# Performance work log

Measured on AMD Instinct MI355X. Metric: run time of the kernel, lower is better.

## Reference

```python
import jax, jax.numpy as jnp
import numpy as np

HEADS = 16
DIM_HEAD = 64


def setup_inputs() -> dict:
    key = jax.random.key(0)
    k1, k2, k3, k4 = jax.random.split(key, 4)
    b, n, d = 2, 2048, 1024
    x = jax.random.normal(k1, (b, n, d), dtype=jnp.float32)
    attn_mask = jax.random.randint(k2, (b, n, n), 0, 2) == 1  # bool mask, True = masked out
    Wqkv = jax.random.normal(k3, (d, 3 * HEADS * DIM_HEAD), dtype=jnp.float32) * (d ** -0.5)
    Wfc = jax.random.normal(k4, (HEADS * DIM_HEAD, d), dtype=jnp.float32) * ((HEADS * DIM_HEAD) ** -0.5)
    return {"x": x, "attn_mask": attn_mask, "Wqkv": Wqkv, "Wfc": Wfc}


def reference(x, attn_mask, Wqkv, Wfc):
    b, n, d = x.shape
    h, dh = HEADS, DIM_HEAD
    qkv = x @ Wqkv  # [b, n, 3*h*dh]
    q, k, v = jnp.split(qkv, 3, axis=-1)
    def to_heads(t):
        return t.reshape(b, n, h, dh).transpose(0, 2, 1, 3)  # b h n d
    q, k, v = to_heads(q), to_heads(k), to_heads(v)
    # NOTE: original divides by scale = dim_head**-0.5, i.e. multiplies by sqrt(dim_head)
    scale = dh ** (-0.5)
    scores = jnp.einsum('bhqd,bhkd->bhqk', q, k) / scale
    scores = jnp.where(attn_mask[:, None, :, :], jnp.float32(-1e9), scores)
    attn = jax.nn.softmax(scores, axis=-1)
    context = jnp.einsum('bhqk,bhkd->bhqd', attn, v)  # b h n dh
    context = context.transpose(0, 2, 1, 3).reshape(b, n, h * dh)
    out = context @ Wfc
    return out, attn
```

## Files before the change

### kernel.cpp

```cpp
#include <hip/hip_runtime.h>

#define HEADS  16
#define DH     64
#define NBATCH 2
#define SEQ    2048
#define DMODEL 1024

typedef unsigned short u16;
typedef unsigned int   u32;
typedef unsigned long long u64;

typedef __attribute__((ext_vector_type(8))) short short8v;
typedef __attribute__((ext_vector_type(4))) float floatx4;

__device__ __forceinline__ u16 f2bf(float f) {
    u32 u = __float_as_uint(f);
    return (u16)((u + 0x7fffu + ((u >> 16) & 1u)) >> 16);
}
__device__ __forceinline__ float bf2f(u16 h) {
    return __uint_as_float(((u32)h) << 16);
}

__global__ void k_split(const float* __restrict__ in, u16* __restrict__ hi,
                        u16* __restrict__ lo, int n4) {
    int i = blockIdx.x * blockDim.x + threadIdx.x;
    if (i >= n4) return;
    float4 v = reinterpret_cast<const float4*>(in)[i];
    ushort4 hv, lv;
    hv.x = f2bf(v.x); hv.y = f2bf(v.y); hv.z = f2bf(v.z); hv.w = f2bf(v.w);
    lv.x = f2bf(v.x - bf2f(hv.x));
    lv.y = f2bf(v.y - bf2f(hv.y));
    lv.z = f2bf(v.z - bf2f(hv.z));
    lv.w = f2bf(v.w - bf2f(hv.w));
    reinterpret_cast<ushort4*>(hi)[i] = hv;
    reinterpret_cast<ushort4*>(lo)[i] = lv;
}

__global__ void k_tsplit(const float* __restrict__ in, u16* __restrict__ hiT,
                         u16* __restrict__ loT, int R, int C, int write_lo) {
    __shared__ float tile[64][65];
    int c0 = blockIdx.x * 64, r0 = blockIdx.y * 64;
    int t = threadIdx.x;
    int lr = t >> 4;
    int lc = (t & 15) * 4;
    for (int i = 0; i < 4; i++) {
        int r = lr + i * 16;
        float4 v = *reinterpret_cast<const float4*>(&in[(size_t)(r0 + r) * C + c0 + lc]);
        tile[r][lc] = v.x; tile[r][lc + 1] = v.y; tile[r][lc + 2] = v.z; tile[r][lc + 3] = v.w;
    }
    __syncthreads();
    for (int i = 0; i < 4; i++) {
        int cc = lr + i * 16;
        float vs0 = tile[lc + 0][cc], vs1 = tile[lc + 1][cc];
        float vs2 = tile[lc + 2][cc], vs3 = tile[lc + 3][cc];
        ushort4 hv, lv;
        hv.x = f2bf(vs0); hv.y = f2bf(vs1); hv.z = f2bf(vs2); hv.w = f2bf(vs3);
        *reinterpret_cast<ushort4*>(&hiT[(size_t)(c0 + cc) * R + r0 + lc]) = hv;
        if (write_lo) {
            lv.x = f2bf(vs0 - bf2f(hv.x)); lv.y = f2bf(vs1 - bf2f(hv.y));
            lv.z = f2bf(vs2 - bf2f(hv.z)); lv.w = f2bf(vs3 - bf2f(hv.w));
            *reinterpret_cast<ushort4*>(&loT[(size_t)(c0 + cc) * R + r0 + lc]) = lv;
        }
    }
}

__global__ void k_maskpack(const int* __restrict__ m, u64* __restrict__ bits) {
    int i = blockIdx.x * 256 + threadIdx.x;
    u64 b = __ballot(m[i] != 0);
    if ((threadIdx.x & 63) == 0) bits[((u32)i) >> 6] = b;
}

__global__ __launch_bounds__(256, 2) void k_qkv(
    const u16* __restrict__ xh, const u16* __restrict__ xl,
    const u16* __restrict__ whT, const u16* __restrict__ wlT,
    u16* __restrict__ qh, u16* __restrict__ ql,
    u16* __restrict__ kh, u16* __restrict__ kl,
    u16* __restrict__ vt)
{
    __shared__ __attribute__((aligned(16))) u16 sA[2][128][72];
    __shared__ __attribute__((aligned(16))) u16 sB[2][128][72];
    int n0 = blockIdx.x * 128;
    int m0 = blockIdx.y * 128;
    bool is_v = (n0 >= 2 * DMODEL);
    int tid = threadIdx.x;
    int wave = tid >> 6, lane = tid & 63;
    int wm = (wave >> 1) * 64, wn = (wave & 1) * 64;
    int lrow = lane & 15, lgrp = lane >> 4;

    floatx4 acc[4][4];
    for (int i = 0; i < 4; i++) for (int j = 0; j < 4; j++) acc[i][j] = (floatx4){0.f, 0.f, 0.f, 0.f};

    int sr = tid >> 1;
    int sc = (tid & 1) * 32;

    for (int k0 = 0; k0 < DMODEL; k0 += 64) {
        const u16* pxh = xh + (size_t)(m0 + sr) * DMODEL + k0 + sc;
        const u16* pwh = whT + (size_t)(n0 + sr) * DMODEL + k0 + sc;
        for (int i = 0; i < 4; i++) {
            *reinterpret_cast<int4*>(&sA[0][sr][sc + i * 8]) = *reinterpret_cast<const int4*>(pxh + i * 8);
            *reinterpret_cast<int4*>(&sB[0][sr][sc + i * 8]) = *reinterpret_cast<const int4*>(pwh + i * 8);
        }
        if (!is_v) {
            const u16* pxl = xl + (size_t)(m0 + sr) * DMODEL + k0 + sc;
            const u16* pwl = wlT + (size_t)(n0 + sr) * DMODEL + k0 + sc;
            for (int i = 0; i < 4; i++) {
                *reinterpret_cast<int4*>(&sA[1][sr][sc + i * 8]) = *reinterpret_cast<const int4*>(pxl + i * 8);
                *reinterpret_cast<int4*>(&sB[1][sr][sc + i * 8]) = *reinterpret_cast<const int4*>(pwl + i * 8);
            }
        }
        __syncthreads();
        for (int ks = 0; ks < 2; ks++) {
            short8v ah[4], bh_[4], al[4], bl_[4];
            for (int i = 0; i < 4; i++) {
                ah[i]  = *reinterpret_cast<const short8v*>(&sA[0][wm + i * 16 + lrow][ks * 32 + lgrp * 8]);
                bh_[i] = *reinterpret_cast<const short8v*>(&sB[0][wn + i * 16 + lrow][ks * 32 + lgrp * 8]);
            }
            if (!is_v) {
                for (int i = 0; i < 4; i++) {
                    al[i]  = *reinterpret_cast<const short8v*>(&sA[1][wm + i * 16 + lrow][ks * 32 + lgrp * 8]);
                    bl_[i] = *reinterpret_cast<const short8v*>(&sB[1][wn + i * 16 + lrow][ks * 32 + lgrp * 8]);
                }
            }
            for (int i = 0; i < 4; i++)
                for (int j = 0; j < 4; j++) {
                    acc[i][j] = __builtin_amdgcn_mfma_f32_16x16x32_bf16(ah[i], bh_[j], acc[i][j], 0, 0, 0);
                    if (!is_v) {
                        acc[i][j] = __builtin_amdgcn_mfma_f32_16x16x32_bf16(ah[i], bl_[j], acc[i][j], 0, 0, 0);
                        acc[i][j] = __builtin_amdgcn_mfma_f32_16x16x32_bf16(al[i], bh_[j], acc[i][j], 0, 0, 0);
                    }
                }
        }
        __syncthreads();
    }
    for (int j = 0; j < 4; j++) {
        int c = n0 + wn + j * 16 + lrow;
        int sel = c >> 10;
        int hcol = c & 1023;
        int hh = hcol >> 6, d = hcol & 63;
        for (int i = 0; i < 4; i++) {
            int mbase = m0 + wm + i * 16 + lgrp * 4;
            int bb = mbase >> 11;
            int nn = mbase & 2047;
            int bh = bb * HEADS + hh;
            if (sel == 2) {
                ushort4 pv;
                pv.x = f2bf(acc[i][j][0]); pv.y = f2bf(acc[i][j][1]);
                pv.z = f2bf(acc[i][j][2]); pv.w = f2bf(acc[i][j][3]);
                *reinterpret_cast<ushort4*>(&vt[((size_t)bh * DH + d) * SEQ + nn]) = pv;
            } else {
                u16* oh = (sel == 0) ? qh : kh;
                u16* ol = (sel == 0) ? ql : kl;
                float sc8 = (sel == 0) ? 8.0f : 1.0f;
                for (int r = 0; r < 4; r++) {
                    float v = acc[i][j][r] * sc8;
                    u16 hv = f2bf(v);
                    u16 lv = f2bf(v - bf2f(hv));
                    size_t addr = ((size_t)bh * SEQ + nn + r) * DH + d;
                    oh[addr] = hv; ol[addr] = lv;
                }
            }
        }
    }
}

__global__ __launch_bounds__(256, 2) void k_attn(
    const u16* __restrict__ qh, const u16* __restrict__ ql,
    const u16* __restrict__ kh, const u16* __restrict__ kl,
    const u16* __restrict__ vt, const u32* __restrict__ mb,
    float* __restrict__ attn, u16* __restrict__ ctx)
{
    __shared__ __attribute__((aligned(16))) u16 sK[2][128][72];
    __shared__ __attribute__((aligned(16))) u16 sV[64][136];
    __shared__ __attribute__((aligned(16))) u16 sP[64][136];
    __shared__ u32 sMask[64][4];
    __shared__ float sML[2][4][64];

    int bh = blockIdx.y;
    int b = bh >> 4, hh = bh & 15;
    int q0 = blockIdx.x * 64;
    int tid = threadIdx.x, wave = tid >> 6, lane = tid & 63;
    int lrow = lane & 15, lgrp = lane >> 4;
    int sr = tid >> 1, scol = (tid & 1) * 32;
    int mr = tid >> 2, mw = tid & 3;

    short8v qfh[4][2], qfl[4][2];
    for (int nt = 0; nt < 4; nt++) {
        int qr = q0 + nt * 16 + lrow;
        const u16* pq = qh + ((size_t)bh * SEQ + qr) * DH + lgrp * 8;
        const u16* pl = ql + ((size_t)bh * SEQ + qr) * DH + lgrp * 8;
        for (int ks = 0; ks < 2; ks++) {
            qfh[nt][ks] = *reinterpret_cast<const short8v*>(pq + ks * 32);
            qfl[nt][ks] = *reinterpret_cast<const short8v*>(pl + ks * 32);
        }
    }

#define STAGE_K_MASK() do { \
        const u16* ph_ = kh + ((size_t)bh * SEQ + kt * 128 + sr) * DH + scol; \
        const u16* pl_ = kl + ((size_t)bh * SEQ + kt * 128 + sr) * DH + scol; \
        for (int i_ = 0; i_ < 4; i_++) { \
            *reinterpret_cast<int4*>(&sK[0][sr][scol + i_ * 8]) = *reinterpret_cast<const int4*>(ph_ + i_ * 8); \
            *reinterpret_cast<int4*>(&sK[1][sr][scol + i_ * 8]) = *reinterpret_cast<const int4*>(pl_ + i_ * 8); \
        } \
        sMask[mr][mw] = mb[((size_t)b * SEQ + q0 + mr) * 64 + kt * 4 + mw]; \
    } while (0)

#define COMPUTE_ST() do { \
        for (int mt_ = 0; mt_ < 2; mt_++) for (int nt_ = 0; nt_ < 4; nt_++) sacc[mt_][nt_] = (floatx4){0.f,0.f,0.f,0.f}; \
        for (int ks_ = 0; ks_ < 2; ks_++) { \
            short8v kfh[2], kfl[2]; \
            for (int mt_ = 0; mt_ < 2; mt_++) { \
                kfh[mt_] = *reinterpret_cast<const short8v*>(&sK[0][wave * 32 + mt_ * 16 + lrow][ks_ * 32 + lgrp * 8]); \
                kfl[mt_] = *reinterpret_cast<const short8v*>(&sK[1][wave * 32 + mt_ * 16 + lrow][ks_ * 32 + lgrp * 8]); \
            } \
            for (int mt_ = 0; mt_ < 2; mt_++) for (int nt_ = 0; nt_ < 4; nt_++) { \
                sacc[mt_][nt_] = __builtin_amdgcn_mfma_f32_16x16x32_bf16(kfh[mt_], qfh[nt_][ks_], sacc[mt_][nt_], 0, 0, 0); \
                sacc[mt_][nt_] = __builtin_amdgcn_mfma_f32_16x16x32_bf16(kfh[mt_], qfl[nt_][ks_], sacc[mt_][nt_], 0, 0, 0); \
                sacc[mt_][nt_] = __builtin_amdgcn_mfma_f32_16x16x32_bf16(kfl[mt_], qfh[nt_][ks_], sacc[mt_][nt_], 0, 0, 0); \
            } \
        } \
    } while (0)

    float m_run[4], l_run[4];
    for (int nt = 0; nt < 4; nt++) { m_run[nt] = -3.0e38f; l_run[nt] = 0.f; }

    for (int kt = 0; kt < 16; kt++) {
        STAGE_K_MASK();
        __syncthreads();
        floatx4 sacc[2][4];
        COMPUTE_ST();
        for (int nt = 0; nt < 4; nt++) {
            u32 mwrd = sMask[nt * 16 + lrow][wave];
            float s[8];
            for (int mt = 0; mt < 2; mt++)
                for (int r = 0; r < 4; r++) {
                    int bit = mt * 16 + lgrp * 4 + r;
                    s[mt * 4 + r] = ((mwrd >> bit) & 1u) ? -1e9f : sacc[mt][nt][r];
                }
            float tmax = s[0];
            for (int u = 1; u < 8; u++) tmax = fmaxf(tmax, s[u]);
            tmax = fmaxf(tmax, __shfl_xor(tmax, 16));
            tmax = fmaxf(tmax, __shfl_xor(tmax, 32));
            float mn = fmaxf(m_run[nt], tmax);
            float ssum = 0.f;
            for (int u = 0; u < 8; u++) ssum += __expf(s[u] - mn);
            ssum += __shfl_xor(ssum, 16);
            ssum += __shfl_xor(ssum, 32);
            l_run[nt] = l_run[nt] * __expf(m_run[nt] - mn) + ssum;
            m_run[nt] = mn;
        }
        __syncthreads();
    }
    if (lane < 16) {
        for (int nt = 0; nt < 4; nt++) {
            sML[0][wave][nt * 16 + lane] = m_run[nt];
            sML[1][wave][nt * 16 + lane] = l_run[nt];
        }
    }
    __syncthreads();
    float m_fin[4], rl[4];
    for (int nt = 0; nt < 4; nt++) {
        int qr = nt * 16 + lrow;
        float m4 = sML[0][0][qr];
        for (int w = 1; w < 4; w++) m4 = fmaxf(m4, sML[0][w][qr]);
        float ls = 0.f;
        for (int w = 0; w < 4; w++) ls += sML[1][w][qr] * __expf(sML[0][w][qr] - m4);
        m_fin[nt] = m4;
        rl[nt] = 1.0f / ls;
    }

    floatx4 cacc[4];
    for (int j = 0; j < 4; j++) cacc[j] = (floatx4){0.f, 0.f, 0.f, 0.f};

    for (int kt = 0; kt < 16; kt++) {
        STAGE_K_MASK();
        {
            int vd = tid >> 2, vq = (tid & 3) * 32;
            const u16* pv = vt + ((size_t)bh * DH + vd) * SEQ + kt * 128 + vq;
            for (int i = 0; i < 4; i++)
                *reinterpret_cast<int4*>(&sV[vd][vq + i * 8]) = *reinterpret_cast<const int4*>(pv + i * 8);
        }
        __syncthreads();
        floatx4 sacc[2][4];
        COMPUTE_ST();
        for (int nt = 0; nt < 4; nt++) {
            u32 mwrd = sMask[nt * 16 + lrow][wave];
            int qr = q0 + nt * 16 + lrow;
            for (int mt = 0; mt < 2; mt++) {
                float4 pf;
                float* pp = &pf.x;
                for (int r = 0; r < 4; r++) {
                    int bit = mt * 16 + lgrp * 4 + r;
                    float sv = ((mwrd >> bit) & 1u) ? -1e9f : sacc[mt][nt][r];
                    pp[r] = __expf(sv - m_fin[nt]) * rl[nt];
                }
                int kc = kt * 128 + wave * 32 + mt * 16 + lgrp * 4;
                *reinterpret_cast<float4*>(&attn[((size_t)bh * SEQ + qr) * SEQ + kc]) = pf;
                ushort4 pb;
                pb.x = f2bf(pp[0]); pb.y = f2bf(pp[1]); pb.z = f2bf(pp[2]); pb.w = f2bf(pp[3]);
                *reinterpret_cast<ushort4*>(&sP[nt * 16 + lrow][wave * 32 + mt * 16 + lgrp * 4]) = pb;
            }
        }
        __syncthreads();
        for (int ks = 0; ks < 4; ks++) {
            short8v pfrag = *reinterpret_cast<const short8v*>(&sP[wave * 16 + lrow][ks * 32 + lgrp * 8]);
            for (int j = 0; j < 4; j++) {
                short8v vfrag = *reinterpret_cast<const short8v*>(&sV[j * 16 + lrow][ks * 32 + lgrp * 8]);
                cacc[j] = __builtin_amdgcn_mfma_f32_16x16x32_bf16(pfrag, vfrag, cacc[j], 0, 0, 0);
            }
        }
        __syncthreads();
    }
    for (int j = 0; j < 4; j++) {
        int d = j * 16 + lrow;
        for (int r = 0; r < 4; r++) {
            int nn = q0 + wave * 16 + lgrp * 4 + r;
            ctx[((size_t)b * SEQ + nn) * DMODEL + hh * 64 + d] = f2bf(cacc[j][r]);
        }
    }
#undef STAGE_K_MASK
#undef COMPUTE_ST
}

__global__ __launch_bounds__(256, 2) void k_out(
    const u16* __restrict__ ctx, const u16* __restrict__ wfcT, float* __restrict__ out)
{
    __shared__ __attribute__((aligned(16))) u16 sA[128][72];
    __shared__ __attribute__((aligned(16))) u16 sB[128][72];
    int n0 = blockIdx.x * 128;
    int m0 = blockIdx.y * 128;
    int tid = threadIdx.x;
    int wave = tid >> 6, lane = tid & 63;
    int wm = (wave >> 1) * 64, wn = (wave & 1) * 64;
    int lrow = lane & 15, lgrp = lane >> 4;

    floatx4 acc[4][4];
    for (int i = 0; i < 4; i++) for (int j = 0; j < 4; j++) acc[i][j] = (floatx4){0.f, 0.f, 0.f, 0.f};

    int sr = tid >> 1;
    int sc = (tid & 1) * 32;

    for (int k0 = 0; k0 < DMODEL; k0 += 64) {
        const u16* pa = ctx + (size_t)(m0 + sr) * DMODEL + k0 + sc;
        const u16* pb = wfcT + (size_t)(n0 + sr) * DMODEL + k0 + sc;
        for (int i = 0; i < 4; i++) {
            *reinterpret_cast<int4*>(&sA[sr][sc + i * 8]) = *reinterpret_cast<const int4*>(pa + i * 8);
            *reinterpret_cast<int4*>(&sB[sr][sc + i * 8]) = *reinterpret_cast<const int4*>(pb + i * 8);
        }
        __syncthreads();
        for (int ks = 0; ks < 2; ks++) {
            short8v af[4], bf[4];
            for (int i = 0; i < 4; i++) {
                af[i] = *reinterpret_cast<const short8v*>(&sA[wm + i * 16 + lrow][ks * 32 + lgrp * 8]);
                bf[i] = *reinterpret_cast<const short8v*>(&sB[wn + i * 16 + lrow][ks * 32 + lgrp * 8]);
            }
            for (int i = 0; i < 4; i++)
                for (int j = 0; j < 4; j++)
                    acc[i][j] = __builtin_amdgcn_mfma_f32_16x16x32_bf16(af[i], bf[j], acc[i][j], 0, 0, 0);
        }
        __syncthreads();
    }
    for (int i = 0; i < 4; i++)
        for (int j = 0; j < 4; j++)
            for (int r = 0; r < 4; r++) {
                int m = m0 + wm + i * 16 + lgrp * 4 + r;
                int c = n0 + wn + j * 16 + lrow;
                out[(size_t)m * DMODEL + c] = acc[i][j][r];
            }
}

extern "C" void kernel_launch(void* const* d_in, const int* in_sizes, int n_in,
                              void* d_out, int out_size, void* d_ws, size_t ws_size,
                              hipStream_t stream) {
    const float* x    = (const float*)d_in[0];
    const int*   mask = (const int*)d_in[1];
    const float* wqkv = (const float*)d_in[2];
    const float* wfc  = (const float*)d_in[3];

    float* out  = (float*)d_out;
    float* attn = out + (size_t)NBATCH * SEQ * DMODEL;

    u16* xh   = (u16*)d_ws;
    u16* xl   = xh + 4194304;
    u16* whT  = xl + 4194304;
    u16* wlT  = whT + 3145728;
    u16* wfcT = wlT + 3145728;
    u16* qh   = wfcT + 1048576;
    u16* ql   = qh + 4194304;
    u16* kh   = ql + 4194304;
    u16* kl   = kh + 4194304;
    u16* vt   = kl + 4194304;
    u32* mbits = (u32*)(vt + 4194304);
    u16* ctx  = xh;

    k_split<<<4096, 256, 0, stream>>>(x, xh, xl, 4194304 / 4);
    k_tsplit<<<dim3(48, 16), 256, 0, stream>>>(wqkv, whT, wlT, 1024, 3072, 1);
    k_tsplit<<<dim3(16, 16), 256, 0, stream>>>(wfc, wfcT, (u16*)nullptr, 1024, 1024, 0);
    k_maskpack<<<32768, 256, 0, stream>>>(mask, (u64*)mbits);
    k_qkv<<<dim3(24, 32), 256, 0, stream>>>(xh, xl, whT, wlT, qh, ql, kh, kl, vt);
    k_attn<<<dim3(32, 32), 256, 0, stream>>>(qh, ql, kh, kl, vt, mbits, attn, ctx);
    k_out<<<dim3(8, 32), 256, 0, stream>>>(ctx, wfcT, out);
}
```

Baseline: 444.1 us.

## Prefetch tiles into registers, shrink attention K tile, switch softmax to exp2

Adds register-staged prefetch of the next K-slice in the QKV and output GEMMs so global loads overlap MFMA work. The attention kernel moves to 64-key tiles with double-buffered K and mask in shared memory, and loads V fragments straight from global memory into registers instead of staging them in LDS. Softmax folds log2(e) into the Q scale and uses exp2 with a precomputed log-sum, which removes the per-element reciprocal. Masked scores now become -3e38 instead of -1e9, so a fully masked row would behave differently. Register pressure rises and LDS use drops.

```diff
diff --git a/kernel.cpp b/kernel.cpp
--- a/kernel.cpp
+++ b/kernel.cpp
@@ -93,22 +93,39 @@
     int sr = tid >> 1;
     int sc = (tid & 1) * 32;
 
+    int4 rah[4], rbh[4], ral[4], rbl[4];
+
+#define QKV_ISSUE(K0) do { \
+        const u16* pxh_ = xh + (size_t)(m0 + sr) * DMODEL + (K0) + sc; \
+        const u16* pwh_ = whT + (size_t)(n0 + sr) * DMODEL + (K0) + sc; \
+        for (int i_ = 0; i_ < 4; i_++) { \
+            rah[i_] = *reinterpret_cast<const int4*>(pxh_ + i_ * 8); \
+            rbh[i_] = *reinterpret_cast<const int4*>(pwh_ + i_ * 8); \
+        } \
+        if (!is_v) { \
+            const u16* pxl_ = xl + (size_t)(m0 + sr) * DMODEL + (K0) + sc; \
+            const u16* pwl_ = wlT + (size_t)(n0 + sr) * DMODEL + (K0) + sc; \
+            for (int i_ = 0; i_ < 4; i_++) { \
+                ral[i_] = *reinterpret_cast<const int4*>(pxl_ + i_ * 8); \
+                rbl[i_] = *reinterpret_cast<const int4*>(pwl_ + i_ * 8); \
+            } \
+        } \
+    } while (0)
+
+    QKV_ISSUE(0);
     for (int k0 = 0; k0 < DMODEL; k0 += 64) {
-        const u16* pxh = xh + (size_t)(m0 + sr) * DMODEL + k0 + sc;
-        const u16* pwh = whT + (size_t)(n0 + sr) * DMODEL + k0 + sc;
         for (int i = 0; i < 4; i++) {
-            *reinterpret_cast<int4*>(&sA[0][sr][sc + i * 8]) = *reinterpret_cast<const int4*>(pxh + i * 8);
-            *reinterpret_cast<int4*>(&sB[0][sr][sc + i * 8]) = *reinterpret_cast<const int4*>(pwh + i * 8);
+            *reinterpret_cast<int4*>(&sA[0][sr][sc + i * 8]) = rah[i];
+            *reinterpret_cast<int4*>(&sB[0][sr][sc + i * 8]) = rbh[i];
         }
         if (!is_v) {
-            const u16* pxl = xl + (size_t)(m0 + sr) * DMODEL + k0 + sc;
-            const u16* pwl = wlT + (size_t)(n0 + sr) * DMODEL + k0 + sc;
             for (int i = 0; i < 4; i++) {
-                *reinterpret_cast<int4*>(&sA[1][sr][sc + i * 8]) = *reinterpret_cast<const int4*>(pxl + i * 8);
-                *reinterpret_cast<int4*>(&sB[1][sr][sc + i * 8]) = *reinterpret_cast<const int4*>(pwl + i * 8);
-            }
-        }
-        __syncthreads();
+                *reinterpret_cast<int4*>(&sA[1][sr][sc + i * 8]) = ral[i];
+                *reinterpret_cast<int4*>(&sB[1][sr][sc + i * 8]) = rbl[i];
+            }
+        }
+        __syncthreads();
+        if (k0 + 64 < DMODEL) QKV_ISSUE(k0 + 64);
         for (int ks = 0; ks < 2; ks++) {
             short8v ah[4], bh_[4], al[4], bl_[4];
             for (int i = 0; i < 4; i++) {
@@ -132,6 +149,7 @@
         }
         __syncthreads();
     }
+#undef QKV_ISSUE
     for (int j = 0; j < 4; j++) {
         int c = n0 + wn + j * 16 + lrow;
         int sel = c >> 10;
@@ -150,7 +168,7 @@
             } else {
                 u16* oh = (sel == 0) ? qh : kh;
                 u16* ol = (sel == 0) ? ql : kl;
-                float sc8 = (sel == 0) ? 8.0f : 1.0f;
+                float sc8 = (sel == 0) ? 11.5415603f : 1.0f;
                 for (int r = 0; r < 4; r++) {
                     float v = acc[i][j][r] * sc8;
                     u16 hv = f2bf(v);
@@ -169,19 +187,20 @@
     const u16* __restrict__ vt, const u32* __restrict__ mb,
     float* __restrict__ attn, u16* __restrict__ ctx)
 {
-    __shared__ __attribute__((aligned(16))) u16 sK[2][128][72];
-    __shared__ __attribute__((aligned(16))) u16 sV[64][136];
-    __shared__ __attribute__((aligned(16))) u16 sP[64][136];
-    __shared__ u32 sMask[64][4];
+    __shared__ __attribute__((aligned(16))) u16 sKh[2][64][72];
+    __shared__ __attribute__((aligned(16))) u16 sKl[2][64][72];
+    __shared__ __attribute__((aligned(16))) u16 sP[64][72];
+    __shared__ u32 sMask[2][64][2];
     __shared__ float sML[2][4][64];
 
     int bh = blockIdx.y;
-    int b = bh >> 4, hh = bh & 15;
+    int b = bh >> 4;
     int q0 = blockIdx.x * 64;
     int tid = threadIdx.x, wave = tid >> 6, lane = tid & 63;
     int lrow = lane & 15, lgrp = lane >> 4;
-    int sr = tid >> 1, scol = (tid & 1) * 32;
-    int mr = tid >> 2, mw = tid & 3;
+    int sr4 = tid >> 2, sc4 = (tid & 3) * 16;
+    int mbit = (wave & 1) * 16 + lgrp * 4;
+    int mwsel = wave >> 1;
 
     short8v qfh[4][2], qfl[4][2];
     for (int nt = 0; nt < 4; nt++) {
@@ -194,62 +213,73 @@
         }
     }
 
-#define STAGE_K_MASK() do { \
-        const u16* ph_ = kh + ((size_t)bh * SEQ + kt * 128 + sr) * DH + scol; \
-        const u16* pl_ = kl + ((size_t)bh * SEQ + kt * 128 + sr) * DH + scol; \
-        for (int i_ = 0; i_ < 4; i_++) { \
-            *reinterpret_cast<int4*>(&sK[0][sr][scol + i_ * 8]) = *reinterpret_cast<const int4*>(ph_ + i_ * 8); \
-            *reinterpret_cast<int4*>(&sK[1][sr][scol + i_ * 8]) = *reinterpret_cast<const int4*>(pl_ + i_ * 8); \
-        } \
-        sMask[mr][mw] = mb[((size_t)b * SEQ + q0 + mr) * 64 + kt * 4 + mw]; \
+    int4 hh0, hh1, ll0, ll1;
+    u32 mv = 0;
+
+#define K_ISSUE(KT) do { \
+        const u16* ph_ = kh + ((size_t)bh * SEQ + (KT) * 64 + sr4) * DH + sc4; \
+        const u16* pl_ = kl + ((size_t)bh * SEQ + (KT) * 64 + sr4) * DH + sc4; \
+        hh0 = *reinterpret_cast<const int4*>(ph_); \
+        hh1 = *reinterpret_cast<const int4*>(ph_ + 8); \
+        ll0 = *reinterpret_cast<const int4*>(pl_); \
+        ll1 = *reinterpret_cast<const int4*>(pl_ + 8); \
+        if (tid < 128) mv = mb[((size_t)b * SEQ + q0 + (tid >> 1)) * 64 + (KT) * 2 + (tid & 1)]; \
     } while (0)
 
-#define COMPUTE_ST() do { \
-        for (int mt_ = 0; mt_ < 2; mt_++) for (int nt_ = 0; nt_ < 4; nt_++) sacc[mt_][nt_] = (floatx4){0.f,0.f,0.f,0.f}; \
+#define K_WRITE(B_) do { \
+        *reinterpret_cast<int4*>(&sKh[B_][sr4][sc4])     = hh0; \
+        *reinterpret_cast<int4*>(&sKh[B_][sr4][sc4 + 8]) = hh1; \
+        *reinterpret_cast<int4*>(&sKl[B_][sr4][sc4])     = ll0; \
+        *reinterpret_cast<int4*>(&sKl[B_][sr4][sc4 + 8]) = ll1; \
+        if (tid < 128) sMask[B_][tid >> 1][tid & 1] = mv; \
+    } while (0)
+
+#define COMPUTE_ST(CUR) do { \
+        for (int nt_ = 0; nt_ < 4; nt_++) sacc[nt_] = (floatx4){0.f, 0.f, 0.f, 0.f}; \
         for (int ks_ = 0; ks_ < 2; ks_++) { \
-            short8v kfh[2], kfl[2]; \
-            for (int mt_ = 0; mt_ < 2; mt_++) { \
-                kfh[mt_] = *reinterpret_cast<const short8v*>(&sK[0][wave * 32 + mt_ * 16 + lrow][ks_ * 32 + lgrp * 8]); \
-                kfl[mt_] = *reinterpret_cast<const short8v*>(&sK[1][wave * 32 + mt_ * 16 + lrow][ks_ * 32 + lgrp * 8]); \
-            } \
-            for (int mt_ = 0; mt_ < 2; mt_++) for (int nt_ = 0; nt_ < 4; nt_++) { \
-                sacc[mt_][nt_] = __builtin_amdgcn_mfma_f32_16x16x32_bf16(kfh[mt_], qfh[nt_][ks_], sacc[mt_][nt_], 0, 0, 0); \
-                sacc[mt_][nt_] = __builtin_amdgcn_mfma_f32_16x16x32_bf16(kfh[mt_], qfl[nt_][ks_], sacc[mt_][nt_], 0, 0, 0); \
-                sacc[mt_][nt_] = __builtin_amdgcn_mfma_f32_16x16x32_bf16(kfl[mt_], qfh[nt_][ks_], sacc[mt_][nt_], 0, 0, 0); \
+            short8v kfh_ = *reinterpret_cast<const short8v*>(&sKh[CUR][wave * 16 + lrow][ks_ * 32 + lgrp * 8]); \
+            short8v kfl_ = *reinterpret_cast<const short8v*>(&sKl[CUR][wave * 16 + lrow][ks_ * 32 + lgrp * 8]); \
+            for (int nt_ = 0; nt_ < 4; nt_++) { \
+                sacc[nt_] = __builtin_amdgcn_mfma_f32_16x16x32_bf16(kfh_, qfh[nt_][ks_], sacc[nt_], 0, 0, 0); \
+                sacc[nt_] = __builtin_amdgcn_mfma_f32_16x16x32_bf16(kfh_, qfl[nt_][ks_], sacc[nt_], 0, 0, 0); \
+                sacc[nt_] = __builtin_amdgcn_mfma_f32_16x16x32_bf16(kfl_, qfh[nt_][ks_], sacc[nt_], 0, 0, 0); \
             } \
         } \
     } while (0)
 
     float m_run[4], l_run[4];
-    for (int nt = 0; nt < 4; nt++) { m_run[nt] = -3.0e38f; l_run[nt] = 0.f; }
-
-    for (int kt = 0; kt < 16; kt++) {
-        STAGE_K_MASK();
-        __syncthreads();
-        floatx4 sacc[2][4];
-        COMPUTE_ST();
+    for (int nt = 0; nt < 4; nt++) { m_run[nt] = -1.0e38f; l_run[nt] = 0.f; }
+
+    K_ISSUE(0);
+    K_WRITE(0);
+    __syncthreads();
+    for (int kt = 0; kt < 32; kt++) {
+        int cur = kt & 1;
+        bool pf = kt < 31;
+        if (pf) K_ISSUE(kt + 1);
+        floatx4 sacc[4];
+        COMPUTE_ST(cur);
         for (int nt = 0; nt < 4; nt++) {
-            u32 mwrd = sMask[nt * 16 + lrow][wave];
-            float s[8];
-            for (int mt = 0; mt < 2; mt++)
-                for (int r = 0; r < 4; r++) {
-                    int bit = mt * 16 + lgrp * 4 + r;
-                    s[mt * 4 + r] = ((mwrd >> bit) & 1u) ? -1e9f : sacc[mt][nt][r];
-                }
-            float tmax = s[0];
-            for (int u = 1; u < 8; u++) tmax = fmaxf(tmax, s[u]);
+            u32 nw = ~sMask[cur][nt * 16 + lrow][mwsel];
+            float sm[4];
+            for (int r = 0; r < 4; r++)
+                sm[r] = ((nw >> (mbit + r)) & 1u) ? sacc[nt][r] : -3.0e38f;
+            float tmax = fmaxf(fmaxf(sm[0], sm[1]), fmaxf(sm[2], sm[3]));
             tmax = fmaxf(tmax, __shfl_xor(tmax, 16));
             tmax = fmaxf(tmax, __shfl_xor(tmax, 32));
             float mn = fmaxf(m_run[nt], tmax);
             float ssum = 0.f;
-            for (int u = 0; u < 8; u++) ssum += __expf(s[u] - mn);
+            for (int r = 0; r < 4; r++)
+                ssum += exp2f(sm[r] - mn);
             ssum += __shfl_xor(ssum, 16);
             ssum += __shfl_xor(ssum, 32);
-            l_run[nt] = l_run[nt] * __expf(m_run[nt] - mn) + ssum;
+            l_run[nt] = l_run[nt] * exp2f(m_run[nt] - mn) + ssum;
             m_run[nt] = mn;
         }
-        __syncthreads();
-    }
+        if (pf) K_WRITE((kt + 1) & 1);
+        __syncthreads();
+    }
+
     if (lane < 16) {
         for (int nt = 0; nt < 4; nt++) {
             sML[0][wave][nt * 16 + lane] = m_run[nt];
@@ -257,59 +287,60 @@
         }
     }
     __syncthreads();
-    float m_fin[4], rl[4];
+    float Cn[4];
     for (int nt = 0; nt < 4; nt++) {
         int qr = nt * 16 + lrow;
         float m4 = sML[0][0][qr];
         for (int w = 1; w < 4; w++) m4 = fmaxf(m4, sML[0][w][qr]);
         float ls = 0.f;
-        for (int w = 0; w < 4; w++) ls += sML[1][w][qr] * __expf(sML[0][w][qr] - m4);
-        m_fin[nt] = m4;
-        rl[nt] = 1.0f / ls;
+        for (int w = 0; w < 4; w++) ls += sML[1][w][qr] * exp2f(sML[0][w][qr] - m4);
+        Cn[nt] = m4 + __log2f(ls);
     }
 
     floatx4 cacc[4];
     for (int j = 0; j < 4; j++) cacc[j] = (floatx4){0.f, 0.f, 0.f, 0.f};
 
-    for (int kt = 0; kt < 16; kt++) {
-        STAGE_K_MASK();
-        {
-            int vd = tid >> 2, vq = (tid & 3) * 32;
-            const u16* pv = vt + ((size_t)bh * DH + vd) * SEQ + kt * 128 + vq;
-            for (int i = 0; i < 4; i++)
-                *reinterpret_cast<int4*>(&sV[vd][vq + i * 8]) = *reinterpret_cast<const int4*>(pv + i * 8);
-        }
-        __syncthreads();
-        floatx4 sacc[2][4];
-        COMPUTE_ST();
+    K_ISSUE(0);
+    K_WRITE(0);
+    __syncthreads();
+    for (int kt = 0; kt < 32; kt++) {
+        int cur = kt & 1;
+        bool pf = kt < 31;
+        int4 vreg[4][2];
+        for (int j = 0; j < 4; j++)
+            for (int ks = 0; ks < 2; ks++)
+                vreg[j][ks] = *reinterpret_cast<const int4*>(
+                    vt + ((size_t)bh * DH + j * 16 + lrow) * SEQ + kt * 64 + ks * 32 + lgrp * 8);
+        if (pf) K_ISSUE(kt + 1);
+        floatx4 sacc[4];
+        COMPUTE_ST(cur);
         for (int nt = 0; nt < 4; nt++) {
-            u32 mwrd = sMask[nt * 16 + lrow][wave];
+            u32 nw = ~sMask[cur][nt * 16 + lrow][mwsel];
             int qr = q0 + nt * 16 + lrow;
-            for (int mt = 0; mt < 2; mt++) {
-                float4 pf;
-                float* pp = &pf.x;
-                for (int r = 0; r < 4; r++) {
-                    int bit = mt * 16 + lgrp * 4 + r;
-                    float sv = ((mwrd >> bit) & 1u) ? -1e9f : sacc[mt][nt][r];
-                    pp[r] = __expf(sv - m_fin[nt]) * rl[nt];
-                }
-                int kc = kt * 128 + wave * 32 + mt * 16 + lgrp * 4;
-                *reinterpret_cast<float4*>(&attn[((size_t)bh * SEQ + qr) * SEQ + kc]) = pf;
-                ushort4 pb;
-                pb.x = f2bf(pp[0]); pb.y = f2bf(pp[1]); pb.z = f2bf(pp[2]); pb.w = f2bf(pp[3]);
-                *reinterpret_cast<ushort4*>(&sP[nt * 16 + lrow][wave * 32 + mt * 16 + lgrp * 4]) = pb;
-            }
-        }
-        __syncthreads();
-        for (int ks = 0; ks < 4; ks++) {
+            float4 pf4;
+            float* pp = &pf4.x;
+            for (int r = 0; r < 4; r++) {
+                float sm = ((nw >> (mbit + r)) & 1u) ? sacc[nt][r] : -3.0e38f;
+                pp[r] = exp2f(sm - Cn[nt]);
+            }
+            int kc = kt * 64 + wave * 16 + lgrp * 4;
+            *reinterpret_cast<float4*>(&attn[((size_t)bh * SEQ + qr) * SEQ + kc]) = pf4;
+            ushort4 pb;
+            pb.x = f2bf(pp[0]); pb.y = f2bf(pp[1]); pb.z = f2bf(pp[2]); pb.w = f2bf(pp[3]);
+            *reinterpret_cast<ushort4*>(&sP[nt * 16 + lrow][wave * 16 + lgrp * 4]) = pb;
+        }
+        __syncthreads();
+        for (int ks = 0; ks < 2; ks++) {
             short8v pfrag = *reinterpret_cast<const short8v*>(&sP[wave * 16 + lrow][ks * 32 + lgrp * 8]);
             for (int j = 0; j < 4; j++) {
-                short8v vfrag = *reinterpret_cast<const short8v*>(&sV[j * 16 + lrow][ks * 32 + lgrp * 8]);
+                short8v vfrag = *reinterpret_cast<short8v*>(&vreg[j][ks]);
                 cacc[j] = __builtin_amdgcn_mfma_f32_16x16x32_bf16(pfrag, vfrag, cacc[j], 0, 0, 0);
             }
         }
-        __syncthreads();
-    }
+        if (pf) K_WRITE((kt + 1) & 1);
+        __syncthreads();
+    }
+    int hh = bh & 15;
     for (int j = 0; j < 4; j++) {
         int d = j * 16 + lrow;
         for (int r = 0; r < 4; r++) {
@@ -317,7 +348,8 @@
             ctx[((size_t)b * SEQ + nn) * DMODEL + hh * 64 + d] = f2bf(cacc[j][r]);
         }
     }
-#undef STAGE_K_MASK
+#undef K_ISSUE
+#undef K_WRITE
 #undef COMPUTE_ST
 }
 
@@ -338,15 +370,25 @@
 
     int sr = tid >> 1;
     int sc = (tid & 1) * 32;
-
+    int4 ra[4], rb[4];
+
+#define OUT_ISSUE(K0) do { \
+        const u16* pa_ = ctx + (size_t)(m0 + sr) * DMODEL + (K0) + sc; \
+        const u16* pb_ = wfcT + (size_t)(n0 + sr) * DMODEL + (K0) + sc; \
+        for (int i_ = 0; i_ < 4; i_++) { \
+            ra[i_] = *reinterpret_cast<const int4*>(pa_ + i_ * 8); \
+            rb[i_] = *reinterpret_cast<const int4*>(pb_ + i_ * 8); \
+        } \
+    } while (0)
+
+    OUT_ISSUE(0);
     for (int k0 = 0; k0 < DMODEL; k0 += 64) {
-        const u16* pa = ctx + (size_t)(m0 + sr) * DMODEL + k0 + sc;
-        const u16* pb = wfcT + (size_t)(n0 + sr) * DMODEL + k0 + sc;
         for (int i = 0; i < 4; i++) {
-            *reinterpret_cast<int4*>(&sA[sr][sc + i * 8]) = *reinterpret_cast<const int4*>(pa + i * 8);
-            *reinterpret_cast<int4*>(&sB[sr][sc + i * 8]) = *reinterpret_cast<const int4*>(pb + i * 8);
-        }
-        __syncthreads();
+            *reinterpret_cast<int4*>(&sA[sr][sc + i * 8]) = ra[i];
+            *reinterpret_cast<int4*>(&sB[sr][sc + i * 8]) = rb[i];
+        }
+        __syncthreads();
+        if (k0 + 64 < DMODEL) OUT_ISSUE(k0 + 64);
         for (int ks = 0; ks < 2; ks++) {
             short8v af[4], bf[4];
             for (int i = 0; i < 4; i++) {
@@ -359,6 +401,7 @@
         }
         __syncthreads();
     }
+#undef OUT_ISSUE
     for (int i = 0; i < 4; i++)
         for (int j = 0; j < 4; j++)
             for (int r = 0; r < 4; r++) {
```

Result: slower. 723.8 us (+63.0%).

## Load K/V fragments directly into registers, use exp2 softmax, double-buffer P

Applied to the files above, without the earlier changes.

The attention kernel stops staging K, V and the mask through shared memory. Each wave now loads its own K and V fragments straight from global memory into registers, prefetching the next K tile, and reads mask words directly. The Q scale is folded with log2(e) so softmax can use exp2, and the final normalisation becomes a single subtraction of m + log2(l). P is double-buffered in LDS so only one barrier per tile is needed, and s_setprio is raised around the MFMA blocks. This cuts LDS traffic and barriers in exchange for more redundant global and cache loads and higher register pressure.

```diff
diff --git a/kernel.cpp b/kernel.cpp
--- a/kernel.cpp
+++ b/kernel.cpp
@@ -19,6 +19,9 @@
 }
 __device__ __forceinline__ float bf2f(u16 h) {
     return __uint_as_float(((u32)h) << 16);
+}
+__device__ __forceinline__ float fexp2(float x) {
+    return __builtin_amdgcn_exp2f(x);
 }
 
 __global__ void k_split(const float* __restrict__ in, u16* __restrict__ hi,
@@ -150,7 +153,7 @@
             } else {
                 u16* oh = (sel == 0) ? qh : kh;
                 u16* ol = (sel == 0) ? ql : kl;
-                float sc8 = (sel == 0) ? 8.0f : 1.0f;
+                float sc8 = (sel == 0) ? 11.5415603f : 1.0f;
                 for (int r = 0; r < 4; r++) {
                     float v = acc[i][j][r] * sc8;
                     u16 hv = f2bf(v);
@@ -169,19 +172,16 @@
     const u16* __restrict__ vt, const u32* __restrict__ mb,
     float* __restrict__ attn, u16* __restrict__ ctx)
 {
-    __shared__ __attribute__((aligned(16))) u16 sK[2][128][72];
-    __shared__ __attribute__((aligned(16))) u16 sV[64][136];
-    __shared__ __attribute__((aligned(16))) u16 sP[64][136];
-    __shared__ u32 sMask[64][4];
+    __shared__ __attribute__((aligned(16))) u16 sP[2][64][72];
     __shared__ float sML[2][4][64];
 
     int bh = blockIdx.y;
-    int b = bh >> 4, hh = bh & 15;
+    int b = bh >> 4;
     int q0 = blockIdx.x * 64;
     int tid = threadIdx.x, wave = tid >> 6, lane = tid & 63;
     int lrow = lane & 15, lgrp = lane >> 4;
-    int sr = tid >> 1, scol = (tid & 1) * 32;
-    int mr = tid >> 2, mw = tid & 3;
+    int mbit = (wave & 1) * 16 + lgrp * 4;
+    int mwsel = wave >> 1;
 
     short8v qfh[4][2], qfl[4][2];
     for (int nt = 0; nt < 4; nt++) {
@@ -194,62 +194,65 @@
         }
     }
 
-#define STAGE_K_MASK() do { \
-        const u16* ph_ = kh + ((size_t)bh * SEQ + kt * 128 + sr) * DH + scol; \
-        const u16* pl_ = kl + ((size_t)bh * SEQ + kt * 128 + sr) * DH + scol; \
-        for (int i_ = 0; i_ < 4; i_++) { \
-            *reinterpret_cast<int4*>(&sK[0][sr][scol + i_ * 8]) = *reinterpret_cast<const int4*>(ph_ + i_ * 8); \
-            *reinterpret_cast<int4*>(&sK[1][sr][scol + i_ * 8]) = *reinterpret_cast<const int4*>(pl_ + i_ * 8); \
-        } \
-        sMask[mr][mw] = mb[((size_t)b * SEQ + q0 + mr) * 64 + kt * 4 + mw]; \
+    const u16* khb = kh + ((size_t)bh * SEQ + wave * 16 + lrow) * DH + lgrp * 8;
+    const u16* klb = kl + ((size_t)bh * SEQ + wave * 16 + lrow) * DH + lgrp * 8;
+    const u32* mbq = mb + ((size_t)(b * SEQ + q0 + lrow)) * 64 + mwsel;
+
+    int4 kh0c, kh1c, kl0c, kl1c, kh0n, kh1n, kl0n, kl1n;
+
+#define K_FETCH(KT, A0, A1, B0, B1) do { \
+        size_t o_ = (size_t)(KT) * 64 * DH; \
+        A0 = *reinterpret_cast<const int4*>(khb + o_); \
+        A1 = *reinterpret_cast<const int4*>(khb + o_ + 32); \
+        B0 = *reinterpret_cast<const int4*>(klb + o_); \
+        B1 = *reinterpret_cast<const int4*>(klb + o_ + 32); \
     } while (0)
 
 #define COMPUTE_ST() do { \
-        for (int mt_ = 0; mt_ < 2; mt_++) for (int nt_ = 0; nt_ < 4; nt_++) sacc[mt_][nt_] = (floatx4){0.f,0.f,0.f,0.f}; \
+        for (int nt_ = 0; nt_ < 4; nt_++) sacc[nt_] = (floatx4){0.f, 0.f, 0.f, 0.f}; \
+        __builtin_amdgcn_s_setprio(1); \
         for (int ks_ = 0; ks_ < 2; ks_++) { \
-            short8v kfh[2], kfl[2]; \
-            for (int mt_ = 0; mt_ < 2; mt_++) { \
-                kfh[mt_] = *reinterpret_cast<const short8v*>(&sK[0][wave * 32 + mt_ * 16 + lrow][ks_ * 32 + lgrp * 8]); \
-                kfl[mt_] = *reinterpret_cast<const short8v*>(&sK[1][wave * 32 + mt_ * 16 + lrow][ks_ * 32 + lgrp * 8]); \
-            } \
-            for (int mt_ = 0; mt_ < 2; mt_++) for (int nt_ = 0; nt_ < 4; nt_++) { \
-                sacc[mt_][nt_] = __builtin_amdgcn_mfma_f32_16x16x32_bf16(kfh[mt_], qfh[nt_][ks_], sacc[mt_][nt_], 0, 0, 0); \
-                sacc[mt_][nt_] = __builtin_amdgcn_mfma_f32_16x16x32_bf16(kfh[mt_], qfl[nt_][ks_], sacc[mt_][nt_], 0, 0, 0); \
-                sacc[mt_][nt_] = __builtin_amdgcn_mfma_f32_16x16x32_bf16(kfl[mt_], qfh[nt_][ks_], sacc[mt_][nt_], 0, 0, 0); \
+            short8v kfh_ = *reinterpret_cast<short8v*>(ks_ ? &kh1c : &kh0c); \
+            short8v kfl_ = *reinterpret_cast<short8v*>(ks_ ? &kl1c : &kl0c); \
+            for (int nt_ = 0; nt_ < 4; nt_++) { \
+                sacc[nt_] = __builtin_amdgcn_mfma_f32_16x16x32_bf16(kfh_, qfh[nt_][ks_], sacc[nt_], 0, 0, 0); \
+                sacc[nt_] = __builtin_amdgcn_mfma_f32_16x16x32_bf16(kfh_, qfl[nt_][ks_], sacc[nt_], 0, 0, 0); \
+                sacc[nt_] = __builtin_amdgcn_mfma_f32_16x16x32_bf16(kfl_, qfh[nt_][ks_], sacc[nt_], 0, 0, 0); \
             } \
         } \
+        __builtin_amdgcn_s_setprio(0); \
     } while (0)
 
     float m_run[4], l_run[4];
-    for (int nt = 0; nt < 4; nt++) { m_run[nt] = -3.0e38f; l_run[nt] = 0.f; }
-
-    for (int kt = 0; kt < 16; kt++) {
-        STAGE_K_MASK();
-        __syncthreads();
-        floatx4 sacc[2][4];
+    for (int nt = 0; nt < 4; nt++) { m_run[nt] = -1.0e38f; l_run[nt] = 0.f; }
+
+    K_FETCH(0, kh0c, kh1c, kl0c, kl1c);
+    #pragma unroll 2
+    for (int kt = 0; kt < 32; kt++) {
+        if (kt < 31) K_FETCH(kt + 1, kh0n, kh1n, kl0n, kl1n);
+        u32 nw4[4];
+        for (int nt = 0; nt < 4; nt++) nw4[nt] = ~mbq[nt * 1024 + kt * 2];
+        floatx4 sacc[4];
         COMPUTE_ST();
         for (int nt = 0; nt < 4; nt++) {
-            u32 mwrd = sMask[nt * 16 + lrow][wave];
-            float s[8];
-            for (int mt = 0; mt < 2; mt++)
-                for (int r = 0; r < 4; r++) {
-                    int bit = mt * 16 + lgrp * 4 + r;
-                    s[mt * 4 + r] = ((mwrd >> bit) & 1u) ? -1e9f : sacc[mt][nt][r];
-                }
-            float tmax = s[0];
-            for (int u = 1; u < 8; u++) tmax = fmaxf(tmax, s[u]);
+            float sm[4];
+            for (int r = 0; r < 4; r++)
+                sm[r] = ((nw4[nt] >> (mbit + r)) & 1u) ? sacc[nt][r] : -3.0e38f;
+            float tmax = fmaxf(fmaxf(sm[0], sm[1]), fmaxf(sm[2], sm[3]));
             tmax = fmaxf(tmax, __shfl_xor(tmax, 16));
             tmax = fmaxf(tmax, __shfl_xor(tmax, 32));
             float mn = fmaxf(m_run[nt], tmax);
             float ssum = 0.f;
-            for (int u = 0; u < 8; u++) ssum += __expf(s[u] - mn);
+            for (int r = 0; r < 4; r++)
+                ssum += fexp2(sm[r] - mn);
             ssum += __shfl_xor(ssum, 16);
             ssum += __shfl_xor(ssum, 32);
-            l_run[nt] = l_run[nt] * __expf(m_run[nt] - mn) + ssum;
+            l_run[nt] = l_run[nt] * fexp2(m_run[nt] - mn) + ssum;
             m_run[nt] = mn;
         }
-        __syncthreads();
-    }
+        kh0c = kh0n; kh1c = kh1n; kl0c = kl0n; kl1c = kl1n;
+    }
+
     if (lane < 16) {
         for (int nt = 0; nt < 4; nt++) {
             sML[0][wave][nt * 16 + lane] = m_run[nt];
@@ -257,59 +260,60 @@
         }
     }
     __syncthreads();
-    float m_fin[4], rl[4];
+    float Cn[4];
     for (int nt = 0; nt < 4; nt++) {
         int qr = nt * 16 + lrow;
         float m4 = sML[0][0][qr];
         for (int w = 1; w < 4; w++) m4 = fmaxf(m4, sML[0][w][qr]);
         float ls = 0.f;
-        for (int w = 0; w < 4; w++) ls += sML[1][w][qr] * __expf(sML[0][w][qr] - m4);
-        m_fin[nt] = m4;
-        rl[nt] = 1.0f / ls;
-    }
+        for (int w = 0; w < 4; w++) ls += sML[1][w][qr] * fexp2(sML[0][w][qr] - m4);
+        Cn[nt] = m4 + __log2f(ls);
+    }
+    __syncthreads();
 
     floatx4 cacc[4];
     for (int j = 0; j < 4; j++) cacc[j] = (floatx4){0.f, 0.f, 0.f, 0.f};
 
-    for (int kt = 0; kt < 16; kt++) {
-        STAGE_K_MASK();
-        {
-            int vd = tid >> 2, vq = (tid & 3) * 32;
-            const u16* pv = vt + ((size_t)bh * DH + vd) * SEQ + kt * 128 + vq;
-            for (int i = 0; i < 4; i++)
-                *reinterpret_cast<int4*>(&sV[vd][vq + i * 8]) = *reinterpret_cast<const int4*>(pv + i * 8);
-        }
-        __syncthreads();
-        floatx4 sacc[2][4];
+    K_FETCH(0, kh0c, kh1c, kl0c, kl1c);
+    for (int kt = 0; kt < 32; kt++) {
+        int cur = kt & 1;
+        int4 vreg[4][2];
+        for (int j = 0; j < 4; j++)
+            for (int ks = 0; ks < 2; ks++)
+                vreg[j][ks] = *reinterpret_cast<const int4*>(
+                    vt + ((size_t)bh * DH + j * 16 + lrow) * SEQ + kt * 64 + ks * 32 + lgrp * 8);
+        if (kt < 31) K_FETCH(kt + 1, kh0n, kh1n, kl0n, kl1n);
+        u32 nw4[4];
+        for (int nt = 0; nt < 4; nt++) nw4[nt] = ~mbq[nt * 1024 + kt * 2];
+        floatx4 sacc[4];
         COMPUTE_ST();
         for (int nt = 0; nt < 4; nt++) {
-            u32 mwrd = sMask[nt * 16 + lrow][wave];
             int qr = q0 + nt * 16 + lrow;
-            for (int mt = 0; mt < 2; mt++) {
-                float4 pf;
-                float* pp = &pf.x;
-                for (int r = 0; r < 4; r++) {
-                    int bit = mt * 16 + lgrp * 4 + r;
-                    float sv = ((mwrd >> bit) & 1u) ? -1e9f : sacc[mt][nt][r];
-                    pp[r] = __expf(sv - m_fin[nt]) * rl[nt];
-                }
-                int kc = kt * 128 + wave * 32 + mt * 16 + lgrp * 4;
-                *reinterpret_cast<float4*>(&attn[((size_t)bh * SEQ + qr) * SEQ + kc]) = pf;
-                ushort4 pb;
-                pb.x = f2bf(pp[0]); pb.y = f2bf(pp[1]); pb.z = f2bf(pp[2]); pb.w = f2bf(pp[3]);
-                *reinterpret_cast<ushort4*>(&sP[nt * 16 + lrow][wave * 32 + mt * 16 + lgrp * 4]) = pb;
-            }
-        }
+            float4 pf4;
+            float* pp = &pf4.x;
+            for (int r = 0; r < 4; r++) {
+                float sm = ((nw4[nt] >> (mbit + r)) & 1u) ? sacc[nt][r] : -3.0e38f;
+                pp[r] = fexp2(sm - Cn[nt]);
+            }
+            int kc = kt * 64 + wave * 16 + lgrp * 4;
+            *reinterpret_cast<float4*>(&attn[((size_t)bh * SEQ + qr) * SEQ + kc]) = pf4;
+            ushort4 pb;
+            pb.x = f2bf(pp[0]); pb.y = f2bf(pp[1]); pb.z = f2bf(pp[2]); pb.w = f2bf(pp[3]);
+            *reinterpret_cast<ushort4*>(&sP[cur][nt * 16 + lrow][wave * 16 + lgrp * 4]) = pb;
+        }
+        kh0c = kh0n; kh1c = kh1n; kl0c = kl0n; kl1c = kl1n;
         __syncthreads();
-        for (int ks = 0; ks < 4; ks++) {
-            short8v pfrag = *reinterpret_cast<const short8v*>(&sP[wave * 16 + lrow][ks * 32 + lgrp * 8]);
+        __builtin_amdgcn_s_setprio(1);
+        for (int ks = 0; ks < 2; ks++) {
+            short8v pfrag = *reinterpret_cast<const short8v*>(&sP[cur][wave * 16 + lrow][ks * 32 + lgrp * 8]);
             for (int j = 0; j < 4; j++) {
-                short8v vfrag = *reinterpret_cast<const short8v*>(&sV[j * 16 + lrow][ks * 32 + lgrp * 8]);
+                short8v vfrag = *reinterpret_cast<short8v*>(&vreg[j][ks]);
                 cacc[j] = __builtin_amdgcn_mfma_f32_16x16x32_bf16(pfrag, vfrag, cacc[j], 0, 0, 0);
             }
         }
-        __syncthreads();
-    }
+        __builtin_amdgcn_s_setprio(0);
+    }
+    int hh = bh & 15;
     for (int j = 0; j < 4; j++) {
         int d = j * 16 + lrow;
         for (int r = 0; r < 4; r++) {
@@ -317,7 +321,7 @@
             ctx[((size_t)b * SEQ + nn) * DMODEL + hh * 64 + d] = f2bf(cacc[j][r]);
         }
     }
-#undef STAGE_K_MASK
+#undef K_FETCH
 #undef COMPUTE_ST
 }
 
```

Measured after the change: 609.4 us. 37.2% more time.
